# Kernel tuning notes

Hardware: AMD Instinct MI355X
Metric: run time of the kernel (lower is better)

The kernel has to match this reference:

```python
import jax, jax.numpy as jnp
import numpy as np
import math

JULIA_ITERS = 64
ESCAPE_RADIUS = 2.0


def _julia_escape_times(seq_len, c_real, c_imag):
    # Positions mapped to the real segment [-2, 2]; iterate z <- z^2 + c,
    # record (first iteration index where |z| > R) / ITERS, else 1.0.
    x = jnp.linspace(-2.0, 2.0, seq_len)
    zr0 = x
    zi0 = jnp.zeros_like(x)
    escaped0 = jnp.zeros(seq_len, dtype=bool)
    et0 = jnp.ones(seq_len, dtype=x.dtype)
    r2 = ESCAPE_RADIUS * ESCAPE_RADIUS

    def step(carry, it):
        zr, zi, escaped, et = carry
        nzr = zr * zr - zi * zi + c_real
        nzi = 2.0 * zr * zi + c_imag
        # torch breaks out of the loop once escaped -> freeze z afterwards
        zr = jnp.where(escaped, zr, nzr)
        zi = jnp.where(escaped, zi, nzi)
        mag2 = zr * zr + zi * zi
        newly = jnp.logical_and(~escaped, mag2 > r2)
        et = jnp.where(newly, it.astype(et.dtype) / JULIA_ITERS, et)
        escaped = jnp.logical_or(escaped, newly)
        return (zr, zi, escaped, et), None

    (_, _, _, et), _ = jax.lax.scan(step, (zr0, zi0, escaped0, et0), jnp.arange(JULIA_ITERS))
    return et


def setup_inputs() -> dict:
    key = jax.random.key(0)
    kq, kk, kv = jax.random.split(key, 3)
    B, S, D = 4, 8192, 64
    return {
        "query": jax.random.normal(kq, (B, S, D), dtype=jnp.float32),
        "key": jax.random.normal(kk, (B, S, D), dtype=jnp.float32),
        "value": jax.random.normal(kv, (B, S, D), dtype=jnp.float32),
        "julia_c_real": jnp.float32(-0.7),
        "julia_c_imag": jnp.float32(0.27),
        "escape_scale": jnp.float32(1.0),
    }


def reference(query, key, value, julia_c_real, julia_c_imag, escape_scale):
    B, S, D = key.shape
    et = _julia_escape_times(S, julia_c_real, julia_c_imag)            # [S]
    julia_weights = jnp.exp(et * escape_scale)                          # [S]
    bias = jnp.log(julia_weights + 1e-8)                                # [S]
    scores = jnp.einsum("bqd,bkd->bqk", query, key) / math.sqrt(D)     # [B,S,S]
    scores = scores + bias[None, None, :]
    attn = jax.nn.softmax(scores, axis=-1)
    out = jnp.einsum("bqk,bkd->bqd", attn, value)                       # [B,S,D]
    return out  # squeeze(1) is a no-op for S > 1
```

## Files before the change

### kernel.cpp

```cpp
#include <hip/hip_runtime.h>
#include <math.h>

#define S_LEN 8192
#define DHEAD 64
#define NBATCH 4
#define BK 32
#define KIT 64

typedef unsigned short u16;
typedef unsigned int u32;
typedef __attribute__((ext_vector_type(8))) _Float16 half8;
typedef __attribute__((ext_vector_type(2))) __fp16 fp16x2;
typedef __attribute__((ext_vector_type(4))) float f32x4;

union HU8 { int4 i4; half8 h8; u32 w[4]; };
union H2U { fp16x2 h2; u32 w; };
union HU  { _Float16 h; u16 u; };

#if __has_builtin(__builtin_amdgcn_exp2f)
#define EXP2(x) __builtin_amdgcn_exp2f(x)
#else
#define EXP2(x) exp2f(x)
#endif

__device__ __forceinline__ u16 f2h(float f) {
    HU x; x.h = (_Float16)f; return x.u;
}
__device__ __forceinline__ u32 packh2(float a, float b) {
    H2U x; x.h2 = __builtin_amdgcn_cvt_pkrtz(a, b); return x.w;
}

__global__ void prep_kernel(const float* __restrict__ K, const float* __restrict__ V,
                            const float* crp, const float* cip, const float* scp,
                            u16* __restrict__ blob, float* __restrict__ bias2) {
    int bid = blockIdx.x, tid = threadIdx.x;
    if (bid < 1024) {
        int b = bid >> 8, t = bid & 255;
        __shared__ float Kt[32 * 64];
        __shared__ float Vt[32 * 65];
        int row = tid >> 3, c8 = (tid & 7) * 8;
        const float* ks = K + ((size_t)(b * S_LEN + t * 32 + row)) * 64 + c8;
        const float* vs = V + ((size_t)(b * S_LEN + t * 32 + row)) * 64 + c8;
        float4 ka = *(const float4*)ks, kb4 = *(const float4*)(ks + 4);
        float4 va = *(const float4*)vs, vb4 = *(const float4*)(vs + 4);
        *(float4*)&Kt[row * 64 + c8] = ka;
        *(float4*)&Kt[row * 64 + c8 + 4] = kb4;
        float* vr = &Vt[row * 65 + c8];
        vr[0] = va.x; vr[1] = va.y; vr[2] = va.z; vr[3] = va.w;
        vr[4] = vb4.x; vr[5] = vb4.y; vr[6] = vb4.z; vr[7] = vb4.w;
        __syncthreads();

        int j = tid >> 6, lane = tid & 63, low = lane & 15, h = lane >> 4;
        u16* tb = blob + ((size_t)(b * 256 + t)) * 4096;
        {
            int kt = j >> 1, ds = j & 1;
            int krow = 8 * (low >> 2) + 4 * kt + (low & 3);
            const float* src = &Kt[krow * 64 + ds * 32 + h * 8];
            u32 wds[4];
#pragma unroll
            for (int i = 0; i < 4; ++i)
                wds[i] = (u32)f2h(src[2 * i]) | ((u32)f2h(src[2 * i + 1]) << 16);
            *(int4*)(tb + j * 512 + lane * 8) = make_int4(wds[0], wds[1], wds[2], wds[3]);
        }
        {
            int col = j * 16 + low;
            u32 wds[4];
#pragma unroll
            for (int i = 0; i < 4; ++i) {
                float a = Vt[(h * 8 + 2 * i) * 65 + col];
                float c = Vt[(h * 8 + 2 * i + 1) * 65 + col];
                wds[i] = (u32)f2h(a) | ((u32)f2h(c) << 16);
            }
            *(int4*)(tb + 2048 + j * 512 + lane * 8) = make_int4(wds[0], wds[1], wds[2], wds[3]);
        }
    } else {
#pragma clang fp contract(off)
        int i = (bid - 1024) * 256 + tid;
        double cr = (double)crp[0], ci = (double)cip[0], sc = (double)scp[0];
        double step = 4.0 / (double)(S_LEN - 1);
        double x = (i == S_LEN - 1) ? 2.0 : (-2.0 + step * (double)i);
        double zr = x, zi = 0.0, et = 1.0;
        bool esc = false;
        for (int it = 0; it < 64; ++it) {
            double nzr = zr * zr - zi * zi + cr;
            double nzi = 2.0 * zr * zi + ci;
            if (!esc) { zr = nzr; zi = nzi; }
            double m2 = zr * zr + zi * zi;
            if (!esc && m2 > 4.0) { et = (double)it / 64.0; esc = true; }
        }
        double bias = log(exp(et * sc) + 1e-8);
        bias2[i] = (float)(bias * 1.4426950408889634 - 20.0);
    }
}

__global__ __launch_bounds__(256, 2)
void flash_kernel(const float* __restrict__ Q, const u16* __restrict__ blob,
                  const float* __restrict__ bias2, float* __restrict__ Out) {
    __shared__ __align__(16) char smem[17664];

    const int tid = threadIdx.x;
    const int l = tid & 63, low = l & 15, h = l >> 4;
    const int kq = __builtin_amdgcn_readfirstlane(tid >> 6);

    const int bid = blockIdx.x;
    const int batch = bid & 3;
    const int qtile = bid >> 2;
    const int q0 = qtile * 64;

    const float qscale = 0.18033688011112042f;
    half8 qfrag[4][2];
#pragma unroll
    for (int qf = 0; qf < 4; ++qf) {
        const float* qrow = Q + ((size_t)(batch * S_LEN + q0 + qf * 16 + low)) * DHEAD + h * 8;
#pragma unroll
        for (int ds = 0; ds < 2; ++ds) {
            f32x4 a = *(const f32x4*)(qrow + ds * 32);
            f32x4 b = *(const f32x4*)(qrow + ds * 32 + 4);
            HU8 u;
            u.w[0] = packh2(a[0] * qscale, a[1] * qscale);
            u.w[1] = packh2(a[2] * qscale, a[3] * qscale);
            u.w[2] = packh2(b[0] * qscale, b[1] * qscale);
            u.w[3] = packh2(b[2] * qscale, b[3] * qscale);
            qfrag[qf][ds] = u.h8;
        }
    }

    const u16* kvb = blob + ((size_t)(batch * 256 + kq * 64)) * 4096;
    const int loff = l * 8;
    const float* bbase = bias2 + kq * 2048;

    f32x4 o[4][4];
#pragma unroll
    for (int qf = 0; qf < 4; ++qf)
#pragma unroll
        for (int dt = 0; dt < 4; ++dt) o[qf][dt] = (f32x4){0, 0, 0, 0};
    float lsum[4] = {0.f, 0.f, 0.f, 0.f};

    HU8 kf[4];
    f32x4 bvv[2];
    HU8 vf[4];
    HU8 pf[4];
    f32x4 stA[2][4];
    f32x4 stB[2][4];

#pragma unroll
    for (int j = 0; j < 4; ++j) kf[j].i4 = *(const int4*)(kvb + j * 512 + loff);
    bvv[0] = *(const f32x4*)(bbase + h * 8);
    bvv[1] = *(const f32x4*)(bbase + h * 8 + 4);
#pragma unroll
    for (int kt = 0; kt < 2; ++kt) {
        const f32x4 binit = kt ? bvv[1] : bvv[0];
#pragma unroll
        for (int qf = 0; qf < 4; ++qf) {
            f32x4 a = __builtin_amdgcn_mfma_f32_16x16x32_f16(kf[kt * 2].h8, qfrag[qf][0], binit, 0, 0, 0);
            a = __builtin_amdgcn_mfma_f32_16x16x32_f16(kf[kt * 2 + 1].h8, qfrag[qf][1], a, 0, 0, 0);
            stA[kt][qf] = a;
        }
    }
#pragma unroll
    for (int j = 0; j < 4; ++j) kf[j].i4 = *(const int4*)(kvb + 4096 + j * 512 + loff);
    bvv[0] = *(const f32x4*)(bbase + 32 + h * 8);
    bvv[1] = *(const f32x4*)(bbase + 32 + h * 8 + 4);
#pragma unroll
    for (int j = 0; j < 4; ++j) vf[j].i4 = *(const int4*)(kvb + 2048 + j * 512 + loff);

#define BODY(KI, STC, STP)                                                       \
    {                                                                            \
        const u16* tb_ = kvb + (size_t)(KI) * 4096;                              \
        const u16* tn_ = tb_ + 4096;                                             \
        _Pragma("unroll")                                                        \
        for (int kt = 0; kt < 2; ++kt) {                                         \
            const f32x4 binit = kt ? bvv[1] : bvv[0];                            \
            _Pragma("unroll")                                                    \
            for (int qf = 0; qf < 4; ++qf) {                                     \
                f32x4 a = __builtin_amdgcn_mfma_f32_16x16x32_f16(                \
                    kf[kt * 2].h8, qfrag[qf][0], binit, 0, 0, 0);                \
                a = __builtin_amdgcn_mfma_f32_16x16x32_f16(                      \
                    kf[kt * 2 + 1].h8, qfrag[qf][1], a, 0, 0, 0);                \
                STC[kt][qf] = a;                                                 \
            }                                                                    \
        }                                                                        \
        _Pragma("unroll")                                                        \
        for (int j = 0; j < 4; ++j)                                              \
            kf[j].i4 = *(const int4*)(tn_ + j * 512 + loff);                     \
        const float* bpn_ = bbase + ((KI) + 1) * 32 + h * 8;                     \
        bvv[0] = *(const f32x4*)bpn_;                                            \
        bvv[1] = *(const f32x4*)(bpn_ + 4);                                      \
        _Pragma("unroll")                                                        \
        for (int kt = 0; kt < 2; ++kt)                                           \
            _Pragma("unroll")                                                    \
            for (int qf = 0; qf < 4; ++qf) {                                     \
                float p0 = EXP2(STP[kt][qf][0]), p1 = EXP2(STP[kt][qf][1]);      \
                float p2 = EXP2(STP[kt][qf][2]), p3 = EXP2(STP[kt][qf][3]);      \
                lsum[qf] += (p0 + p1) + (p2 + p3);                               \
                pf[qf].w[kt * 2]     = packh2(p0, p1);                           \
                pf[qf].w[kt * 2 + 1] = packh2(p2, p3);                           \
            }                                                                    \
        _Pragma("unroll")                                                        \
        for (int dt = 0; dt < 4; ++dt)                                           \
            _Pragma("unroll")                                                    \
            for (int qf = 0; qf < 4; ++qf)                                       \
                o[qf][dt] = __builtin_amdgcn_mfma_f32_16x16x32_f16(              \
                    vf[dt].h8, pf[qf].h8, o[qf][dt], 0, 0, 0);                   \
        _Pragma("unroll")                                                        \
        for (int j = 0; j < 4; ++j)                                              \
            vf[j].i4 = *(const int4*)(tb_ + 2048 + j * 512 + loff);              \
    }

#pragma unroll 1
    for (int kp = 1; kp < KIT - 1; kp += 2) {
        BODY(kp, stB, stA)
        BODY(kp + 1, stA, stB)
    }
    BODY(KIT - 1, stB, stA)
#undef BODY

#pragma unroll
    for (int kt = 0; kt < 2; ++kt)
#pragma unroll
        for (int qf = 0; qf < 4; ++qf) {
            float p0 = EXP2(stB[kt][qf][0]), p1 = EXP2(stB[kt][qf][1]);
            float p2 = EXP2(stB[kt][qf][2]), p3 = EXP2(stB[kt][qf][3]);
            lsum[qf] += (p0 + p1) + (p2 + p3);
            pf[qf].w[kt * 2]     = packh2(p0, p1);
            pf[qf].w[kt * 2 + 1] = packh2(p2, p3);
        }
#pragma unroll
    for (int dt = 0; dt < 4; ++dt)
#pragma unroll
        for (int qf = 0; qf < 4; ++qf)
            o[qf][dt] = __builtin_amdgcn_mfma_f32_16x16x32_f16(vf[dt].h8, pf[qf].h8, o[qf][dt], 0, 0, 0);

#pragma unroll
    for (int qf = 0; qf < 4; ++qf) {
        lsum[qf] += __shfl_xor(lsum[qf], 16, 64);
        lsum[qf] += __shfl_xor(lsum[qf], 32, 64);
    }

    float* MO = (float*)smem;
    float* ML = (float*)(smem + 17408);
#pragma unroll 1
    for (int src = 1; src < 4; ++src) {
        __syncthreads();
        if (kq == src) {
#pragma unroll
            for (int qf = 0; qf < 4; ++qf) {
                const int row = qf * 16 + low;
#pragma unroll
                for (int dt = 0; dt < 4; ++dt)
                    *(f32x4*)&MO[row * 68 + dt * 16 + h * 4] = o[qf][dt];
                if (h == 0) ML[row] = lsum[qf];
            }
        }
        __syncthreads();
        if (kq == 0) {
#pragma unroll
            for (int qf = 0; qf < 4; ++qf) {
                const int row = qf * 16 + low;
#pragma unroll
                for (int dt = 0; dt < 4; ++dt) {
                    f32x4 a = *(const f32x4*)&MO[row * 68 + dt * 16 + h * 4];
#pragma unroll
                    for (int jj = 0; jj < 4; ++jj) o[qf][dt][jj] += a[jj];
                }
                lsum[qf] += ML[row];
            }
        }
    }

    if (kq == 0) {
#pragma unroll
        for (int qf = 0; qf < 4; ++qf) {
            const float inv = 1.f / lsum[qf];
            float* orow = Out + ((size_t)(batch * S_LEN + q0 + qf * 16 + low)) * DHEAD;
#pragma unroll
            for (int dt = 0; dt < 4; ++dt) {
                f32x4 r;
#pragma unroll
                for (int jj = 0; jj < 4; ++jj) r[jj] = o[qf][dt][jj] * inv;
                *(f32x4*)(orow + dt * 16 + h * 4) = r;
            }
        }
    }
}

extern "C" void kernel_launch(void* const* d_in, const int* in_sizes, int n_in,
                              void* d_out, int out_size, void* d_ws, size_t ws_size,
                              hipStream_t stream) {
    const float* Q  = (const float*)d_in[0];
    const float* K  = (const float*)d_in[1];
    const float* V  = (const float*)d_in[2];
    const float* cr = (const float*)d_in[3];
    const float* ci = (const float*)d_in[4];
    const float* sc = (const float*)d_in[5];
    float* out = (float*)d_out;

    char* ws = (char*)d_ws;
    float* bias2 = (float*)ws;
    u16*   blob  = (u16*)(ws + 33024);

    prep_kernel<<<dim3(1056), dim3(256), 0, stream>>>(K, V, cr, ci, sc, blob, bias2);
    flash_kernel<<<dim3(512), dim3(256), 0, stream>>>(Q, blob, bias2, out);
}
```

Measured before the change: 147.1 us.

## Interleave PV MFMAs with exp of current scores, double-buffer P instead of S

```diff
diff --git a/kernel.cpp b/kernel.cpp
--- a/kernel.cpp
+++ b/kernel.cpp
@@ -139,9 +139,9 @@
     HU8 kf[4];
     f32x4 bvv[2];
     HU8 vf[4];
-    HU8 pf[4];
-    f32x4 stA[2][4];
-    f32x4 stB[2][4];
+    HU8 pfA[4];
+    HU8 pfB[4];
+    f32x4 st[2][4];
 
 #pragma unroll
     for (int j = 0; j < 4; ++j) kf[j].i4 = *(const int4*)(kvb + j * 512 + loff);
@@ -153,8 +153,7 @@
 #pragma unroll
         for (int qf = 0; qf < 4; ++qf) {
             f32x4 a = __builtin_amdgcn_mfma_f32_16x16x32_f16(kf[kt * 2].h8, qfrag[qf][0], binit, 0, 0, 0);
-            a = __builtin_amdgcn_mfma_f32_16x16x32_f16(kf[kt * 2 + 1].h8, qfrag[qf][1], a, 0, 0, 0);
-            stA[kt][qf] = a;
+            st[kt][qf] = __builtin_amdgcn_mfma_f32_16x16x32_f16(kf[kt * 2 + 1].h8, qfrag[qf][1], a, 0, 0, 0);
         }
     }
 #pragma unroll
@@ -162,9 +161,19 @@
     bvv[0] = *(const f32x4*)(bbase + 32 + h * 8);
     bvv[1] = *(const f32x4*)(bbase + 32 + h * 8 + 4);
 #pragma unroll
+    for (int kt = 0; kt < 2; ++kt)
+#pragma unroll
+        for (int qf = 0; qf < 4; ++qf) {
+            float p0 = EXP2(st[kt][qf][0]), p1 = EXP2(st[kt][qf][1]);
+            float p2 = EXP2(st[kt][qf][2]), p3 = EXP2(st[kt][qf][3]);
+            lsum[qf] += (p0 + p1) + (p2 + p3);
+            pfA[qf].w[kt * 2]     = packh2(p0, p1);
+            pfA[qf].w[kt * 2 + 1] = packh2(p2, p3);
+        }
+#pragma unroll
     for (int j = 0; j < 4; ++j) vf[j].i4 = *(const int4*)(kvb + 2048 + j * 512 + loff);
 
-#define BODY(KI, STC, STP)                                                       \
+#define BODY(KI, PFP, PFC)                                                       \
     {                                                                            \
         const u16* tb_ = kvb + (size_t)(KI) * 4096;                              \
         const u16* tn_ = tb_ + 4096;                                             \
@@ -175,9 +184,8 @@
             for (int qf = 0; qf < 4; ++qf) {                                     \
                 f32x4 a = __builtin_amdgcn_mfma_f32_16x16x32_f16(                \
                     kf[kt * 2].h8, qfrag[qf][0], binit, 0, 0, 0);                \
-                a = __builtin_amdgcn_mfma_f32_16x16x32_f16(                      \
+                st[kt][qf] = __builtin_amdgcn_mfma_f32_16x16x32_f16(             \
                     kf[kt * 2 + 1].h8, qfrag[qf][1], a, 0, 0, 0);                \
-                STC[kt][qf] = a;                                                 \
             }                                                                    \
         }                                                                        \
         _Pragma("unroll")                                                        \
@@ -187,21 +195,16 @@
         bvv[0] = *(const f32x4*)bpn_;                                            \
         bvv[1] = *(const f32x4*)(bpn_ + 4);                                      \
         _Pragma("unroll")                                                        \
-        for (int kt = 0; kt < 2; ++kt)                                           \
-            _Pragma("unroll")                                                    \
-            for (int qf = 0; qf < 4; ++qf) {                                     \
-                float p0 = EXP2(STP[kt][qf][0]), p1 = EXP2(STP[kt][qf][1]);      \
-                float p2 = EXP2(STP[kt][qf][2]), p3 = EXP2(STP[kt][qf][3]);      \
-                lsum[qf] += (p0 + p1) + (p2 + p3);                               \
-                pf[qf].w[kt * 2]     = packh2(p0, p1);                           \
-                pf[qf].w[kt * 2 + 1] = packh2(p2, p3);                           \
-            }                                                                    \
-        _Pragma("unroll")                                                        \
-        for (int dt = 0; dt < 4; ++dt)                                           \
-            _Pragma("unroll")                                                    \
-            for (int qf = 0; qf < 4; ++qf)                                       \
-                o[qf][dt] = __builtin_amdgcn_mfma_f32_16x16x32_f16(              \
-                    vf[dt].h8, pf[qf].h8, o[qf][dt], 0, 0, 0);                   \
+        for (int s = 0; s < 16; ++s) {                                           \
+            const int dt = s >> 2, qfp = s & 3;                                  \
+            o[qfp][dt] = __builtin_amdgcn_mfma_f32_16x16x32_f16(                 \
+                vf[dt].h8, PFP[qfp].h8, o[qfp][dt], 0, 0, 0);                    \
+            const int kt = s >> 3, qfs = (s >> 1) & 3, pr = s & 1;               \
+            float pa = EXP2(st[kt][qfs][2 * pr]);                                \
+            float pb = EXP2(st[kt][qfs][2 * pr + 1]);                            \
+            lsum[qfs] += pa + pb;                                                \
+            PFC[qfs].w[kt * 2 + pr] = packh2(pa, pb);                            \
+        }                                                                        \
         _Pragma("unroll")                                                        \
         for (int j = 0; j < 4; ++j)                                              \
             vf[j].i4 = *(const int4*)(tb_ + 2048 + j * 512 + loff);              \
@@ -209,27 +212,17 @@
 
 #pragma unroll 1
     for (int kp = 1; kp < KIT - 1; kp += 2) {
-        BODY(kp, stB, stA)
-        BODY(kp + 1, stA, stB)
-    }
-    BODY(KIT - 1, stB, stA)
+        BODY(kp, pfA, pfB)
+        BODY(kp + 1, pfB, pfA)
+    }
+    BODY(KIT - 1, pfA, pfB)
 #undef BODY
 
 #pragma unroll
-    for (int kt = 0; kt < 2; ++kt)
-#pragma unroll
-        for (int qf = 0; qf < 4; ++qf) {
-            float p0 = EXP2(stB[kt][qf][0]), p1 = EXP2(stB[kt][qf][1]);
-            float p2 = EXP2(stB[kt][qf][2]), p3 = EXP2(stB[kt][qf][3]);
-            lsum[qf] += (p0 + p1) + (p2 + p3);
-            pf[qf].w[kt * 2]     = packh2(p0, p1);
-            pf[qf].w[kt * 2 + 1] = packh2(p2, p3);
-        }
-#pragma unroll
     for (int dt = 0; dt < 4; ++dt)
 #pragma unroll
         for (int qf = 0; qf < 4; ++qf)
-            o[qf][dt] = __builtin_amdgcn_mfma_f32_16x16x32_f16(vf[dt].h8, pf[qf].h8, o[qf][dt], 0, 0, 0);
+            o[qf][dt] = __builtin_amdgcn_mfma_f32_16x16x32_f16(vf[dt].h8, pfB[qf].h8, o[qf][dt], 0, 0, 0);
 
 #pragma unroll
     for (int qf = 0; qf < 4; ++qf) {
```

Result: no change. 148.8 us (+1.1%).

## Split KV range across eight waves per block with tree reduction of partials

Applied to the files above, without the earlier changes.

```diff
diff --git a/kernel.cpp b/kernel.cpp
--- a/kernel.cpp
+++ b/kernel.cpp
@@ -5,7 +5,7 @@
 #define DHEAD 64
 #define NBATCH 4
 #define BK 32
-#define KIT 64
+#define KIT 32
 
 typedef unsigned short u16;
 typedef unsigned int u32;
@@ -93,10 +93,10 @@
     }
 }
 
-__global__ __launch_bounds__(256, 2)
+__global__ __launch_bounds__(512, 2)
 void flash_kernel(const float* __restrict__ Q, const u16* __restrict__ blob,
                   const float* __restrict__ bias2, float* __restrict__ Out) {
-    __shared__ __align__(16) char smem[17664];
+    __shared__ __align__(16) char smem[70656];
 
     const int tid = threadIdx.x;
     const int l = tid & 63, low = l & 15, h = l >> 4;
@@ -125,9 +125,9 @@
         }
     }
 
-    const u16* kvb = blob + ((size_t)(batch * 256 + kq * 64)) * 4096;
+    const u16* kvb = blob + ((size_t)(batch * 256 + kq * KIT)) * 4096;
     const int loff = l * 8;
-    const float* bbase = bias2 + kq * 2048;
+    const float* bbase = bias2 + kq * (KIT * 32);
 
     f32x4 o[4][4];
 #pragma unroll
@@ -163,6 +163,9 @@
     bvv[1] = *(const f32x4*)(bbase + 32 + h * 8 + 4);
 #pragma unroll
     for (int j = 0; j < 4; ++j) vf[j].i4 = *(const int4*)(kvb + 2048 + j * 512 + loff);
+
+    if (kq & 1)        __builtin_amdgcn_s_sleep(5);
+    if ((kq >> 2) & 1) __builtin_amdgcn_s_sleep(11);
 
 #define BODY(KI, STC, STP)                                                       \
     {                                                                            \
@@ -237,36 +240,46 @@
         lsum[qf] += __shfl_xor(lsum[qf], 32, 64);
     }
 
-    float* MO = (float*)smem;
-    float* ML = (float*)(smem + 17408);
-#pragma unroll 1
-    for (int src = 1; src < 4; ++src) {
-        __syncthreads();
-        if (kq == src) {
-#pragma unroll
-            for (int qf = 0; qf < 4; ++qf) {
-                const int row = qf * 16 + low;
-#pragma unroll
-                for (int dt = 0; dt < 4; ++dt)
-                    *(f32x4*)&MO[row * 68 + dt * 16 + h * 4] = o[qf][dt];
-                if (h == 0) ML[row] = lsum[qf];
+    auto wpart = [&](int slot) {
+        float* MO = (float*)(smem + slot * 17664);
+        float* ML = (float*)(smem + slot * 17664 + 17408);
+#pragma unroll
+        for (int qf = 0; qf < 4; ++qf) {
+            const int row = qf * 16 + low;
+#pragma unroll
+            for (int dt = 0; dt < 4; ++dt)
+                *(f32x4*)&MO[row * 68 + dt * 16 + h * 4] = o[qf][dt];
+            if (h == 0) ML[row] = lsum[qf];
+        }
+    };
+    auto apart = [&](int slot) {
+        float* MO = (float*)(smem + slot * 17664);
+        float* ML = (float*)(smem + slot * 17664 + 17408);
+#pragma unroll
+        for (int qf = 0; qf < 4; ++qf) {
+            const int row = qf * 16 + low;
+#pragma unroll
+            for (int dt = 0; dt < 4; ++dt) {
+                f32x4 a = *(const f32x4*)&MO[row * 68 + dt * 16 + h * 4];
+#pragma unroll
+                for (int jj = 0; jj < 4; ++jj) o[qf][dt][jj] += a[jj];
             }
-        }
-        __syncthreads();
-        if (kq == 0) {
-#pragma unroll
-            for (int qf = 0; qf < 4; ++qf) {
-                const int row = qf * 16 + low;
-#pragma unroll
-                for (int dt = 0; dt < 4; ++dt) {
-                    f32x4 a = *(const f32x4*)&MO[row * 68 + dt * 16 + h * 4];
-#pragma unroll
-                    for (int jj = 0; jj < 4; ++jj) o[qf][dt][jj] += a[jj];
-                }
-                lsum[qf] += ML[row];
-            }
-        }
-    }
+            lsum[qf] += ML[row];
+        }
+    };
+
+    __syncthreads();
+    if (kq & 1) wpart(kq >> 1);
+    __syncthreads();
+    if (!(kq & 1)) apart(kq >> 1);
+    __syncthreads();
+    if ((kq & 3) == 2) wpart(kq >> 2);
+    __syncthreads();
+    if ((kq & 3) == 0) apart(kq >> 2);
+    __syncthreads();
+    if (kq == 4) wpart(0);
+    __syncthreads();
+    if (kq == 0) apart(0);
 
     if (kq == 0) {
 #pragma unroll
@@ -300,5 +313,5 @@
     u16*   blob  = (u16*)(ws + 33024);
 
     prep_kernel<<<dim3(1056), dim3(256), 0, stream>>>(K, V, cr, ci, sc, blob, bias2);
-    flash_kernel<<<dim3(512), dim3(256), 0, stream>>>(Q, blob, bias2, out);
-}
+    flash_kernel<<<dim3(512), dim3(512), 0, stream>>>(Q, blob, bias2, out);
+}
```

Measured after the change: 153.8 us. 4.6% more time.
